# Performance work log

Measured on AMD Instinct MI355X. Metric: run time of the kernel, lower is better.

The kernel has to match this reference:

```python
import jax, jax.numpy as jnp
import numpy as np

BN_EPS = 1e-5
SLOPE = 0.01  # LeakyReLU negative slope (torch default)


def setup_inputs() -> dict:
    key = jax.random.key(0)
    ks = jax.random.split(key, 16)
    N, E = 100000, 1600000
    Cin, C, S, L, Lc = 64, 128, 256, 3, 2
    inp = {}
    inp["x"] = jax.random.normal(ks[0], (N, Cin), jnp.float32)
    inp["edge_index"] = jax.random.randint(ks[1], (2, E), 0, N, jnp.int32)
    inp["batch"] = jnp.zeros((N,), jnp.int32)
    # first GIN layer params
    inp["eps1"] = jnp.zeros((1,), jnp.float32)
    inp["W1"] = jax.random.normal(ks[2], (Cin, C), jnp.float32) * (1.0 / np.sqrt(Cin))
    inp["b1"] = jnp.zeros((C,), jnp.float32)
    inp["g1"] = jnp.ones((C,), jnp.float32)
    inp["be1"] = jnp.zeros((C,), jnp.float32)
    inp["m1"] = jnp.zeros((C,), jnp.float32)
    inp["v1"] = jax.random.uniform(ks[3], (C,), jnp.float32, 0.5, 1.5)
    # stacked GIN layers
    inp["epsL"] = jnp.zeros((L,), jnp.float32)
    inp["WL"] = jax.random.normal(ks[4], (L, C, C), jnp.float32) * (1.0 / np.sqrt(C))
    inp["bL"] = jnp.zeros((L, C), jnp.float32)
    inp["gL"] = jnp.ones((L, C), jnp.float32)
    inp["beL"] = jnp.zeros((L, C), jnp.float32)
    inp["mL"] = jnp.zeros((L, C), jnp.float32)
    inp["vL"] = jax.random.uniform(ks[5], (L, C), jnp.float32, 0.5, 1.5)
    # classifier
    inp["Wc1"] = jax.random.normal(ks[6], (C, S), jnp.float32) * (1.0 / np.sqrt(C))
    inp["bc1"] = jnp.zeros((S,), jnp.float32)
    inp["Wcl"] = jax.random.normal(ks[7], (Lc, S, S), jnp.float32) * (1.0 / np.sqrt(S))
    inp["bcl"] = jnp.zeros((Lc, S), jnp.float32)
    inp["Wf"] = jax.random.normal(ks[8], (S, 1), jnp.float32) * (1.0 / np.sqrt(S))
    inp["bf"] = jnp.zeros((1,), jnp.float32)
    return inp


def reference(x, edge_index, batch, eps1, W1, b1, g1, be1, m1, v1,
              epsL, WL, bL, gL, beL, mL, vL, Wc1, bc1, Wcl, bcl, Wf, bf):
    N = x.shape[0]
    src, dst = edge_index[0], edge_index[1]
    lrelu = lambda z: jnp.where(z >= 0, z, SLOPE * z)

    def gin(h, eps, W, b, g, be, m, v):
        # scatter-add neighbor aggregation: aggr[i] = sum_{(j->i) in E} h[j]
        aggr = jax.ops.segment_sum(h[src], dst, num_segments=N)
        z = ((1.0 + eps) * h + aggr) @ W + b          # Linear
        z = (z - m) * (g * jax.lax.rsqrt(v + BN_EPS)) + be  # BatchNorm (inference)
        return lrelu(z)                                # LeakyReLU in MLP; Dropout=identity

    h = lrelu(gin(x, eps1, W1, b1, g1, be1, m1, v1))  # outer leaky_relu in forward
    for i in range(WL.shape[0]):
        h = lrelu(gin(h, epsL[i], WL[i], bL[i], gL[i], beL[i], mL[i], vL[i]))
    h = h @ Wc1 + bc1
    for i in range(Wcl.shape[0]):
        h = lrelu(h @ Wcl[i] + bcl[i])
    return jax.nn.sigmoid(h @ Wf + bf)  # [N, 1]
```

## Files before the change

### kernel.cpp

```cpp
#include <hip/hip_runtime.h>
#include <stdint.h>


#define NN  100000
#define EE  1600000
#define CIN 64
#define CC  128
#define NBK 782
#define CHUNK 8192
#define NCH 196

typedef __attribute__((ext_vector_type(8))) __bf16 bf16x8;
typedef __attribute__((ext_vector_type(4))) float  f32x4;

__device__ __forceinline__ float bf2f(uint32_t u) { return __uint_as_float(u << 16); }
__device__ __forceinline__ float bf2f_hi(uint32_t u) { return __uint_as_float(u & 0xffff0000u); }
__device__ __forceinline__ ushort f2bf(float f) {
  uint32_t u = __float_as_uint(f);
  u += 0x7fffu + ((u >> 16) & 1u);
  return (ushort)(u >> 16);
}

template<int ACT> __device__ __forceinline__ float actf(float z) {
  if constexpr (ACT == 1) return z >= 0.f ? z : 0.01f * z;
  else if constexpr (ACT == 2) return z >= 0.f ? z : 1e-4f * z;
  else return z;
}

__device__ __forceinline__ void gload_lds16(const void* g, void* l) {
  __builtin_amdgcn_global_load_lds(
      (const __attribute__((address_space(1))) void*)g,
      (__attribute__((address_space(3))) void*)l, 16, 0, 0);
}

__global__ __launch_bounds__(256) void ms_hist_kernel(const int* __restrict__ ei,
                                                      int* __restrict__ hist,
                                                      int* __restrict__ bh, int e) {
  __shared__ int h[NBK];
  for (int i = threadIdx.x; i < NBK; i += 256) h[i] = 0;
  __syncthreads();
  const int base = blockIdx.x * CHUNK;
  const int end = min(base + CHUNK, e);
  for (int i = base + threadIdx.x; i < end; i += 256)
    atomicAdd(&h[ei[e + i] >> 7], 1);
  __syncthreads();
  for (int i = threadIdx.x; i < NBK; i += 256) {
    hist[blockIdx.x * NBK + i] = h[i];
    if (h[i]) atomicAdd(&bh[i], h[i]);
  }
}

__global__ __launch_bounds__(256) void bkt_scan_kernel(const int* __restrict__ bh,
                                                       int* __restrict__ boff, int e) {
  __shared__ int sd[256];
  int t = threadIdx.x;
  int base = t * 4;
  int v0 = base + 0 < NBK ? bh[base + 0] : 0;
  int v1 = base + 1 < NBK ? bh[base + 1] : 0;
  int v2 = base + 2 < NBK ? bh[base + 2] : 0;
  int v3 = base + 3 < NBK ? bh[base + 3] : 0;
  int ts = v0 + v1 + v2 + v3;
  sd[t] = ts; __syncthreads();
  for (int off = 1; off < 256; off <<= 1) {
    int u = (t >= off) ? sd[t - off] : 0;
    __syncthreads();
    sd[t] += u;
    __syncthreads();
  }
  int excl = sd[t] - ts;
  if (base + 0 < NBK) boff[base + 0] = excl;
  if (base + 1 < NBK) boff[base + 1] = excl + v0;
  if (base + 2 < NBK) boff[base + 2] = excl + v0 + v1;
  if (base + 3 < NBK) boff[base + 3] = excl + v0 + v1 + v2;
  if (t == 255) boff[NBK] = e;
}

__global__ void ms_offs_kernel(int* __restrict__ hist, const int* __restrict__ boff) {
  int b = blockIdx.x * 256 + threadIdx.x;
  if (b >= NBK) return;
  int run = boff[b];
  for (int k = 0; k < NCH; ++k) {
    int t = hist[k * NBK + b];
    hist[k * NBK + b] = run;
    run += t;
  }
}

__global__ __launch_bounds__(256) void ms_scatter_kernel(const int* __restrict__ ei,
                                                         const int* __restrict__ hist,
                                                         uint* __restrict__ ebkt, int e) {
  __shared__ int cur[NBK];
  for (int i = threadIdx.x; i < NBK; i += 256) cur[i] = hist[blockIdx.x * NBK + i];
  __syncthreads();
  const int base = blockIdx.x * CHUNK;
  const int end = min(base + CHUNK, e);
  for (int i = base + threadIdx.x; i < end; i += 256) {
    int s = ei[i], d = ei[e + i];
    int p = atomicAdd(&cur[d >> 7], 1);
    ebkt[p] = ((uint)(d & 127) << 17) | (uint)s;
  }
}

__global__ __launch_bounds__(256) void bkt_deg_kernel(const uint* __restrict__ ebkt,
                                                      const int* __restrict__ boff,
                                                      int* __restrict__ deg, int n) {
  __shared__ int dl[128];
  int b = blockIdx.x;
  for (int i = threadIdx.x; i < 128; i += 256) dl[i] = 0;
  __syncthreads();
  int j1 = boff[b + 1];
  for (int j = boff[b] + threadIdx.x; j < j1; j += 256)
    atomicAdd(&dl[ebkt[j] >> 17], 1);
  __syncthreads();
  for (int i = threadIdx.x; i < 128; i += 256) {
    int node = (b << 7) + i;
    if (node < n) deg[node] = dl[i];
  }
}

__global__ __launch_bounds__(256) void bkt_fill_kernel(const uint* __restrict__ ebkt,
                                                       const int* __restrict__ boff,
                                                       const int* __restrict__ rowp,
                                                       int* __restrict__ colb, int n) {
  __shared__ int cur[128];
  int b = blockIdx.x;
  for (int i = threadIdx.x; i < 128; i += 256) {
    int node = (b << 7) + i;
    cur[i] = (node < n) ? rowp[node] : 0;
  }
  __syncthreads();
  int j1 = boff[b + 1];
  for (int j = boff[b] + threadIdx.x; j < j1; j += 256) {
    uint v = ebkt[j];
    int p = atomicAdd(&cur[v >> 17], 1);
    colb[p] = (int)(v & 0x1FFFFu);
  }
}

__global__ void scan1_kernel(const int* __restrict__ deg, int* __restrict__ outp,
                             int* __restrict__ partial, int n) {
  __shared__ int sd[256];
  int t = threadIdx.x;
  int base = blockIdx.x * 1024 + t * 4;
  int v0 = base + 0 < n ? deg[base + 0] : 0;
  int v1 = base + 1 < n ? deg[base + 1] : 0;
  int v2 = base + 2 < n ? deg[base + 2] : 0;
  int v3 = base + 3 < n ? deg[base + 3] : 0;
  int ts = v0 + v1 + v2 + v3;
  sd[t] = ts; __syncthreads();
  for (int off = 1; off < 256; off <<= 1) {
    int u = (t >= off) ? sd[t - off] : 0;
    __syncthreads();
    sd[t] += u;
    __syncthreads();
  }
  int excl = sd[t] - ts;
  if (base + 0 < n) outp[base + 0] = excl;
  if (base + 1 < n) outp[base + 1] = excl + v0;
  if (base + 2 < n) outp[base + 2] = excl + v0 + v1;
  if (base + 3 < n) outp[base + 3] = excl + v0 + v1 + v2;
  if (t == 255) partial[blockIdx.x] = sd[255];
}

__global__ void scan2_kernel(int* __restrict__ partial, int nb) {
  __shared__ int sd[256];
  int t = threadIdx.x;
  int v = t < nb ? partial[t] : 0;
  sd[t] = v; __syncthreads();
  for (int off = 1; off < 256; off <<= 1) {
    int u = (t >= off) ? sd[t - off] : 0;
    __syncthreads();
    sd[t] += u;
    __syncthreads();
  }
  if (t < nb) partial[t] = sd[t] - v;
}

__global__ void scan3_kernel(int* __restrict__ rowp, const int* __restrict__ partial,
                             int n, int e) {
  int i = blockIdx.x * 256 + threadIdx.x;
  if (i == 0) rowp[n] = e;
  if (i < n) rowp[i] += partial[i >> 10];
}

__global__ void bnprep_kernel(const float* b1, const float* g1, const float* be1,
                              const float* m1, const float* v1,
                              const float* bL, const float* gL, const float* beL,
                              const float* mL, const float* vL,
                              float* __restrict__ sc, float* __restrict__ tc) {
  int i = blockIdx.x * 256 + threadIdx.x;
  if (i >= 4 * 128) return;
  int layer = i >> 7, c = i & 127;
  float b, g, be, m, v;
  if (layer == 0) { b = b1[c]; g = g1[c]; be = be1[c]; m = m1[c]; v = v1[c]; }
  else { int o = (layer - 1) * 128 + c; b = bL[o]; g = gL[o]; be = beL[o]; m = mL[o]; v = vL[o]; }
  float s = g * rsqrtf(v + 1e-5f);
  sc[i] = s;
  tc[i] = (b - m) * s + be;
}

__global__ void wtprep_kernel(const float* __restrict__ W1, const float* __restrict__ WL,
                              const float* __restrict__ Wc1, const float* __restrict__ Wcl,
                              ushort* __restrict__ wt1, ushort* __restrict__ wtL,
                              ushort* __restrict__ wtc1, ushort* __restrict__ wtcl) {
  int i = blockIdx.x * 256 + threadIdx.x;
  if (i < 8192) {
    int m = i >> 6, k = i & 63;
    wt1[i] = f2bf(W1[k * 128 + m]);
  } else if (i < 8192 + 49152) {
    int j = i - 8192;
    int l = j >> 14, r = j & 16383, m = r >> 7, k = r & 127;
    wtL[j] = f2bf(WL[l * 16384 + k * 128 + m]);
  } else if (i < 8192 + 49152 + 32768) {
    int j = i - (8192 + 49152);
    int m = j >> 7, k = j & 127;
    wtc1[j] = f2bf(Wc1[k * 256 + m]);
  } else if (i < 8192 + 49152 + 32768 + 131072) {
    int j = i - (8192 + 49152 + 32768);
    int l = j >> 16, r = j & 65535, m = r >> 8, k = r & 255;
    wtcl[j] = f2bf(Wcl[l * 65536 + k * 256 + m]);
  }
}

__global__ void xconv_kernel(const float* __restrict__ x, ushort* __restrict__ xb, int n4) {
  int i = blockIdx.x * 256 + threadIdx.x;
  if (i < n4) {
    float4 v = ((const float4*)x)[i];
    ushort4 o;
    o.x = f2bf(v.x); o.y = f2bf(v.y); o.z = f2bf(v.z); o.w = f2bf(v.w);
    ((ushort4*)xb)[i] = o;
  }
}

template<int C>
__global__ __launch_bounds__(256) void agg_kernel(
    const ushort* __restrict__ hb, const int* __restrict__ rowp,
    const int* __restrict__ colb, const float* __restrict__ ep,
    ushort* __restrict__ zout, int n)
{
  constexpr int LPE = C / 8;
  constexpr int EPR = 64 / LPE;
  const int lane = threadIdx.x & 63;
  const int node = blockIdx.x * 4 + (threadIdx.x >> 6);
  if (node >= n) return;
  const float e1 = 1.0f + ep[0];
  const int lo = lane & (LPE - 1);
  const int g  = lane / LPE;
  int j0 = rowp[node], jend = rowp[node + 1];

  float a0 = 0.f, a1 = 0.f, a2 = 0.f, a3 = 0.f,
        a4 = 0.f, a5 = 0.f, a6 = 0.f, a7 = 0.f;

  for (; j0 < jend; j0 += 64) {
    int cnt = jend - j0; if (cnt > 64) cnt = 64;
    int myn = (lane < cnt) ? colb[j0 + lane] : 0;
    int rounds = (cnt + EPR - 1) / EPR;
    #pragma unroll 4
    for (int r = 0; r < rounds; ++r) {
      int e = r * EPR + g;
      int u = __shfl(myn, e);
      if (e < cnt) {
        const uint4 v = *(const uint4*)(hb + (size_t)u * C + lo * 8);
        a0 += bf2f(v.x); a1 += bf2f_hi(v.x);
        a2 += bf2f(v.y); a3 += bf2f_hi(v.y);
        a4 += bf2f(v.z); a5 += bf2f_hi(v.z);
        a6 += bf2f(v.w); a7 += bf2f_hi(v.w);
      }
    }
  }

  #pragma unroll
  for (int s = LPE; s < 64; s <<= 1) {
    a0 += __shfl_xor(a0, s); a1 += __shfl_xor(a1, s);
    a2 += __shfl_xor(a2, s); a3 += __shfl_xor(a3, s);
    a4 += __shfl_xor(a4, s); a5 += __shfl_xor(a5, s);
    a6 += __shfl_xor(a6, s); a7 += __shfl_xor(a7, s);
  }

  if (g == 0) {
    const uint4 d = *(const uint4*)(hb + (size_t)node * C + lo * 8);
    uint4 o;
    o.x = (uint)f2bf(e1 * bf2f(d.x) + a0) | ((uint)f2bf(e1 * bf2f_hi(d.x) + a1) << 16);
    o.y = (uint)f2bf(e1 * bf2f(d.y) + a2) | ((uint)f2bf(e1 * bf2f_hi(d.y) + a3) << 16);
    o.z = (uint)f2bf(e1 * bf2f(d.z) + a4) | ((uint)f2bf(e1 * bf2f_hi(d.z) + a5) << 16);
    o.w = (uint)f2bf(e1 * bf2f(d.w) + a6) | ((uint)f2bf(e1 * bf2f_hi(d.w) + a7) << 16);
    *(uint4*)(zout + (size_t)node * C + lo * 8) = o;
  }
}

template<int K, int M, int ACT, bool BN>
__global__ __launch_bounds__(256) void gemm_kernel(
    const ushort* __restrict__ xin,
    const ushort* __restrict__ wt,
    const float*  __restrict__ sc,
    const float*  __restrict__ tc,
    ushort* __restrict__ hout,
    int n)
{
  constexpr int KS = 64;
  __shared__ ushort ldsW[128 * KS];
  __shared__ ushort ldsX[128 * KS];
  const int tid = threadIdx.x;
  const int wave = tid >> 6, lane = tid & 63;
  const int lr = lane & 15, lg = lane >> 4;
  const int n0 = blockIdx.x * 128;
  const int mB = blockIdx.y * 128;

  f32x4 acc[8][2];
  #pragma unroll
  for (int r = 0; r < 8; ++r) {
    acc[r][0] = (f32x4){0.f, 0.f, 0.f, 0.f};
    acc[r][1] = (f32x4){0.f, 0.f, 0.f, 0.f};
  }

  #pragma unroll
  for (int s = 0; s < K / KS; ++s) {
    if (s) __syncthreads();
    #pragma unroll
    for (int i = 0; i < 4; ++i) {
      const int ub = wave * 4096 + i * 1024;
      const int a  = ub + lane * 16;
      const int m  = a >> 7;
      const int o  = (a & 127) ^ ((m & 7) << 4);
      gload_lds16((const char*)wt + ((size_t)(mB + m) * K) * 2 + s * 128 + o,
                  (char*)ldsW + ub);
      int nd = n0 + m; if (nd >= n) nd = n - 1;
      gload_lds16((const char*)xin + ((size_t)nd * K) * 2 + s * 128 + o,
                  (char*)ldsX + ub);
    }
    asm volatile("s_waitcnt vmcnt(0)" ::: "memory");
    __syncthreads();
    #pragma unroll
    for (int k0 = 0; k0 < KS; k0 += 32) {
      const int kb = (k0 + lg * 8) * 2;
      bf16x8 wf0, wf1;
      {
        int m = wave * 32 + lr;
        wf0 = __builtin_bit_cast(bf16x8,
              *(const uint4*)((const char*)ldsW + ((m * 128 + kb) ^ ((m & 7) << 4))));
        m += 16;
        wf1 = __builtin_bit_cast(bf16x8,
              *(const uint4*)((const char*)ldsW + ((m * 128 + kb) ^ ((m & 7) << 4))));
      }
      #pragma unroll
      for (int r = 0; r < 8; ++r) {
        int xr = r * 16 + lr;
        bf16x8 xf = __builtin_bit_cast(bf16x8,
              *(const uint4*)((const char*)ldsX + ((xr * 128 + kb) ^ ((xr & 7) << 4))));
        acc[r][0] = __builtin_amdgcn_mfma_f32_16x16x32_bf16(wf0, xf, acc[r][0], 0, 0, 0);
        acc[r][1] = __builtin_amdgcn_mfma_f32_16x16x32_bf16(wf1, xf, acc[r][1], 0, 0, 0);
      }
    }
  }

  #pragma unroll
  for (int ct = 0; ct < 2; ++ct) {
    const int c0 = mB + wave * 32 + ct * 16 + lg * 4;
    float4 sv;
    if constexpr (BN) sv = *(const float4*)(sc + c0);
    else sv = make_float4(1.f, 1.f, 1.f, 1.f);
    const float4 tv = *(const float4*)(tc + c0);
    #pragma unroll
    for (int r = 0; r < 8; ++r) {
      const int node = n0 + r * 16 + lr;
      if (node < n) {
        const f32x4 a = acc[r][ct];
        ushort4 o;
        o.x = f2bf(actf<ACT>(a[0] * sv.x + tv.x));
        o.y = f2bf(actf<ACT>(a[1] * sv.y + tv.y));
        o.z = f2bf(actf<ACT>(a[2] * sv.z + tv.z));
        o.w = f2bf(actf<ACT>(a[3] * sv.w + tv.w));
        *(ushort4*)(hout + (size_t)node * M + c0) = o;
      }
    }
  }
}

__global__ __launch_bounds__(512) void cls_kernel(
    const ushort* __restrict__ xin,
    const ushort* __restrict__ wc1,
    const float*  __restrict__ bc1,
    const ushort* __restrict__ wcl,
    const float*  __restrict__ bcl,
    const float*  __restrict__ wfv,
    const float*  __restrict__ bfp,
    float* __restrict__ out, int n)
{
  extern __shared__ char lds[];
  char* ldsW0 = lds;
  char* ldsW1 = lds + 32768;
  char* ldsH  = lds + 65536;
  char* ldsX  = lds + 131072;
  const int tid = threadIdx.x;
  const int wave = tid >> 6, lane = tid & 63;
  const int lr = lane & 15, lg = lane >> 4;
  const int n0 = blockIdx.x * 128;

  f32x4 acc[8][2];

  auto stageW = [&](const ushort* wsrc, int K2, int s, char* dst) {
    #pragma unroll
    for (int i = 0; i < 4; ++i) {
      const int ub = wave * 4096 + i * 1024;
      const int a = ub + lane * 16;
      const int m = a >> 7;
      const int o = (a & 127) ^ ((m & 7) << 4);
      gload_lds16((const char*)wsrc + (size_t)m * K2 * 2 + s * 128 + o, dst + ub);
    }
  };
  auto stageX = [&](int s) {
    #pragma unroll
    for (int i = 0; i < 2; ++i) {
      const int ub = wave * 2048 + i * 1024;
      const int a = ub + lane * 16;
      const int m = a >> 7;
      const int o = (a & 127) ^ ((m & 7) << 4);
      int nd = n0 + m; if (nd >= n) nd = n - 1;
      gload_lds16((const char*)xin + (size_t)nd * 128 * 2 + s * 128 + o, ldsX + ub);
    }
  };
  auto mfma_slab = [&](const char* wbuf, const char* xbase, int rowOff) {
    #pragma unroll
    for (int k0 = 0; k0 < 64; k0 += 32) {
      const int kb = (k0 + lg * 8) * 2;
      bf16x8 wfr[2];
      #pragma unroll
      for (int ct = 0; ct < 2; ++ct) {
        int m = wave * 32 + ct * 16 + lr;
        wfr[ct] = __builtin_bit_cast(bf16x8,
                  *(const uint4*)(wbuf + ((m * 128 + kb) ^ ((m & 7) << 4))));
      }
      #pragma unroll
      for (int r = 0; r < 8; ++r) {
        int xr = rowOff + r * 16 + lr;
        bf16x8 xf = __builtin_bit_cast(bf16x8,
                    *(const uint4*)(xbase + ((xr * 128 + kb) ^ ((xr & 7) << 4))));
        #pragma unroll
        for (int ct = 0; ct < 2; ++ct)
          acc[r][ct] = __builtin_amdgcn_mfma_f32_16x16x32_bf16(wfr[ct], xf, acc[r][ct], 0, 0, 0);
      }
    }
  };
  auto zacc = [&]() {
    #pragma unroll
    for (int r = 0; r < 8; ++r)
      #pragma unroll
      for (int c = 0; c < 2; ++c) acc[r][c] = (f32x4){0.f, 0.f, 0.f, 0.f};
  };
  auto writeH = [&](const float* bias, bool act) {
    #pragma unroll
    for (int ct = 0; ct < 2; ++ct) {
      const int c0 = wave * 32 + ct * 16 + lg * 4;
      const float4 bv = *(const float4*)(bias + c0);
      const int slab = c0 >> 6, cis = (c0 & 63) * 2;
      #pragma unroll
      for (int r = 0; r < 8; ++r) {
        const int rowH = slab * 128 + r * 16 + lr;
        const f32x4 a = acc[r][ct];
        ushort4 o;
        if (act) {
          o.x = f2bf(actf<1>(a[0] + bv.x)); o.y = f2bf(actf<1>(a[1] + bv.y));
          o.z = f2bf(actf<1>(a[2] + bv.z)); o.w = f2bf(actf<1>(a[3] + bv.w));
        } else {
          o.x = f2bf(a[0] + bv.x); o.y = f2bf(a[1] + bv.y);
          o.z = f2bf(a[2] + bv.z); o.w = f2bf(a[3] + bv.w);
        }
        *(ushort4*)(ldsH + ((rowH * 128 + cis) ^ ((rowH & 7) << 4))) = o;
      }
    }
  };

  zacc();
  #pragma unroll
  for (int s = 0; s < 2; ++s) {
    if (s) __syncthreads();
    stageX(s);
    stageW(wc1, 128, s, ldsW0);
    asm volatile("s_waitcnt vmcnt(0)" ::: "memory");
    __syncthreads();
    mfma_slab(ldsW0, ldsX, 0);
  }
  __syncthreads();
  writeH(bc1, false);

  for (int g = 0; g < 2; ++g) {
    const ushort* Wg = wcl + g * 65536;
    const float*  bg = bcl + g * 256;
    zacc();
    __syncthreads();
    stageW(Wg, 256, 0, ldsW0);
    #pragma unroll
    for (int s = 0; s < 4; ++s) {
      char* cur = (s & 1) ? ldsW1 : ldsW0;
      char* nxt = (s & 1) ? ldsW0 : ldsW1;
      if (s + 1 < 4) {
        stageW(Wg, 256, s + 1, nxt);
        asm volatile("s_waitcnt vmcnt(4)" ::: "memory");
      } else {
        asm volatile("s_waitcnt vmcnt(0)" ::: "memory");
      }
      __syncthreads();
      mfma_slab(cur, ldsH, s * 128);
      __syncthreads();
    }
    if (g == 0) {
      writeH(bg, true);
    } else {
      float* red = (float*)ldsX;
      #pragma unroll
      for (int r = 0; r < 8; ++r) {
        float p = 0.f;
        #pragma unroll
        for (int ct = 0; ct < 2; ++ct) {
          const int c0 = wave * 32 + ct * 16 + lg * 4;
          const float4 bv = *(const float4*)(bg + c0);
          const float4 wv = *(const float4*)(wfv + c0);
          const f32x4 a = acc[r][ct];
          p += actf<1>(a[0] + bv.x) * wv.x + actf<1>(a[1] + bv.y) * wv.y
             + actf<1>(a[2] + bv.z) * wv.z + actf<1>(a[3] + bv.w) * wv.w;
        }
        p += __shfl_xor(p, 16);
        p += __shfl_xor(p, 32);
        if (lg == 0) red[wave * 128 + r * 16 + lr] = p;
      }
      __syncthreads();
      if (tid < 128) {
        const int nd = n0 + tid;
        if (nd < n) {
          float logit = bfp[0];
          #pragma unroll
          for (int w = 0; w < 8; ++w) logit += red[w * 128 + tid];
          out[nd] = 1.f / (1.f + expf(-logit));
        }
      }
    }
  }
}

extern "C" void kernel_launch(void* const* d_in, const int* in_sizes, int n_in,
                              void* d_out, int out_size, void* d_ws, size_t ws_size,
                              hipStream_t stream)
{
  const float* x    = (const float*)d_in[0];
  const int*   ei   = (const int*)d_in[1];
  const float* eps1 = (const float*)d_in[3];
  const float* W1   = (const float*)d_in[4];
  const float* b1   = (const float*)d_in[5];
  const float* g1   = (const float*)d_in[6];
  const float* be1  = (const float*)d_in[7];
  const float* m1   = (const float*)d_in[8];
  const float* v1   = (const float*)d_in[9];
  const float* epsL = (const float*)d_in[10];
  const float* WL   = (const float*)d_in[11];
  const float* bL   = (const float*)d_in[12];
  const float* gL   = (const float*)d_in[13];
  const float* beL  = (const float*)d_in[14];
  const float* mL   = (const float*)d_in[15];
  const float* vL   = (const float*)d_in[16];
  const float* Wc1  = (const float*)d_in[17];
  const float* bc1  = (const float*)d_in[18];
  const float* Wcl  = (const float*)d_in[19];
  const float* bcl  = (const float*)d_in[20];
  const float* Wf   = (const float*)d_in[21];
  const float* bfp  = (const float*)d_in[22];
  float* out = (float*)d_out;

  char* w = (char*)d_ws;
  size_t off = 0;
  auto alloc = [&](size_t bytes) {
    char* p = w + off;
    off += (bytes + 255) & ~(size_t)255;
    return p;
  };
  ushort* bufA   = (ushort*)alloc((size_t)NN * 256 * 2);
  ushort* bufB   = (ushort*)alloc((size_t)NN * 256 * 2);
  int*    rowp   = (int*)alloc((NN + 1) * 4);
  int*    deg    = (int*)alloc(NN * 4);
  int*    colb   = (int*)alloc((size_t)EE * 4);
  uint*   ebkt   = (uint*)alloc((size_t)EE * 4);
  int*    hist   = (int*)alloc((size_t)NCH * NBK * 4);
  int*    bh     = (int*)alloc(NBK * 4);
  int*    boff   = (int*)alloc((NBK + 1) * 4);
  int*    partial= (int*)alloc(1024);
  ushort* wt1    = (ushort*)alloc(8192 * 2);
  ushort* wtL    = (ushort*)alloc(49152 * 2);
  ushort* wtc1   = (ushort*)alloc(32768 * 2);
  ushort* wtcl   = (ushort*)alloc(131072 * 2);
  float*  sc     = (float*)alloc(512 * 4);
  float*  tc     = (float*)alloc(512 * 4);
  (void)ws_size; (void)in_sizes; (void)n_in; (void)out_size;

  hipMemsetAsync(bh, 0, NBK * 4, stream);
  ms_hist_kernel<<<NCH, 256, 0, stream>>>(ei, hist, bh, EE);
  bkt_scan_kernel<<<1, 256, 0, stream>>>(bh, boff, EE);
  ms_offs_kernel<<<(NBK + 255) / 256, 256, 0, stream>>>(hist, boff);
  ms_scatter_kernel<<<NCH, 256, 0, stream>>>(ei, hist, ebkt, EE);
  bkt_deg_kernel<<<NBK, 256, 0, stream>>>(ebkt, boff, deg, NN);
  scan1_kernel<<<98, 256, 0, stream>>>(deg, rowp, partial, NN);
  scan2_kernel<<<1, 256, 0, stream>>>(partial, 98);
  scan3_kernel<<<(NN + 255) / 256, 256, 0, stream>>>(rowp, partial, NN, EE);
  bkt_fill_kernel<<<NBK, 256, 0, stream>>>(ebkt, boff, rowp, colb, NN);

  bnprep_kernel<<<2, 256, 0, stream>>>(b1, g1, be1, m1, v1, bL, gL, beL, mL, vL, sc, tc);
  wtprep_kernel<<<864, 256, 0, stream>>>(W1, WL, Wc1, Wcl, wt1, wtL, wtc1, wtcl);
  xconv_kernel<<<(NN * CIN / 4 + 255) / 256, 256, 0, stream>>>(x, bufA, NN * CIN / 4);

  const int GB = (NN + 127) / 128;

  agg_kernel<64><<<25000, 256, 0, stream>>>(bufA, rowp, colb, eps1, bufB, NN);
  gemm_kernel<64, 128, 2, true><<<dim3(GB, 1), 256, 0, stream>>>(bufB, wt1, sc, tc, bufA, NN);
  for (int i = 0; i < 3; ++i) {
    agg_kernel<128><<<25000, 256, 0, stream>>>(bufA, rowp, colb, epsL + i, bufB, NN);
    gemm_kernel<128, 128, 2, true><<<dim3(GB, 1), 256, 0, stream>>>(
        bufB, wtL + i * 16384, sc + 128 * (i + 1), tc + 128 * (i + 1), bufA, NN);
  }
  hipFuncSetAttribute(reinterpret_cast<const void*>(cls_kernel),
                      hipFuncAttributeMaxDynamicSharedMemorySize, 147456);
  cls_kernel<<<GB, 512, 147456, stream>>>(bufA, wtc1, bc1, wtcl, bcl, Wf, bfp, out, NN);
}
```

Measured before the change: 455.0 us.

## Store node features in FP8 (bf8) for neighbor aggregation gathers

Node feature tensors that feed the gather-based aggregation are now stored in 8-bit bf8 (e5m2) format instead of bf16. This halves the bytes per random neighbor gather. The input conversion and the GEMM epilogues write bf8, and the aggregation decodes it with hardware packed conversions when available. The final GIN layer still writes bf16 for the classifier. The cost is a large loss of precision (a 2-bit mantissa) on the activations, which may break accuracy tolerance.

```diff
diff --git a/kernel.cpp b/kernel.cpp
--- a/kernel.cpp
+++ b/kernel.cpp
@@ -1,4 +1,5 @@
 #include <hip/hip_runtime.h>
+#include <hip/hip_fp16.h>
 #include <stdint.h>
 
 
@@ -12,6 +13,7 @@
 
 typedef __attribute__((ext_vector_type(8))) __bf16 bf16x8;
 typedef __attribute__((ext_vector_type(4))) float  f32x4;
+typedef __attribute__((ext_vector_type(2))) float  f32x2;
 
 __device__ __forceinline__ float bf2f(uint32_t u) { return __uint_as_float(u << 16); }
 __device__ __forceinline__ float bf2f_hi(uint32_t u) { return __uint_as_float(u & 0xffff0000u); }
@@ -19,6 +21,35 @@
   uint32_t u = __float_as_uint(f);
   u += 0x7fffu + ((u >> 16) & 1u);
   return (ushort)(u >> 16);
+}
+
+#if __has_builtin(__builtin_amdgcn_cvt_pk_f32_bf8) && __has_builtin(__builtin_amdgcn_cvt_pk_bf8_f32)
+#define F8_HW 1
+#endif
+
+template<bool HI> __device__ __forceinline__ f32x2 dec_pk(uint d) {
+#ifdef F8_HW
+  return __builtin_amdgcn_cvt_pk_f32_bf8((int)d, HI);
+#else
+  uint w = HI ? (d >> 16) : d;
+  f32x2 r;
+  uint b0 = w & 0xFFu, b1 = (w >> 8) & 0xFFu;
+  r.x = __uint_as_float(((b0 & 0x80u) << 24) | ((b0 & 0x7Fu) << 21)) * 0x1.0p112f;
+  r.y = __uint_as_float(((b1 & 0x80u) << 24) | ((b1 & 0x7Fu) << 21)) * 0x1.0p112f;
+  return r;
+#endif
+}
+template<bool HI> __device__ __forceinline__ uint enc_pk(float a, float b, uint old) {
+#ifdef F8_HW
+  return (uint)__builtin_amdgcn_cvt_pk_bf8_f32(a, b, (int)old, HI);
+#else
+  ushort ha = __half_as_ushort(__float2half(a));
+  ushort hb = __half_as_ushort(__float2half(b));
+  ha = (ushort)(ha + 0x7F + ((ha >> 8) & 1));
+  hb = (ushort)(hb + 0x7F + ((hb >> 8) & 1));
+  uint two = (uint)(ha >> 8) | ((uint)(hb >> 8) << 8);
+  return HI ? ((old & 0x0000FFFFu) | (two << 16)) : ((old & 0xFFFF0000u) | two);
+#endif
 }
 
 template<int ACT> __device__ __forceinline__ float actf(float z) {
@@ -222,23 +253,23 @@
   }
 }
 
-__global__ void xconv_kernel(const float* __restrict__ x, ushort* __restrict__ xb, int n4) {
+__global__ void xconv_kernel(const float* __restrict__ x, uchar* __restrict__ x8, int n4) {
   int i = blockIdx.x * 256 + threadIdx.x;
   if (i < n4) {
     float4 v = ((const float4*)x)[i];
-    ushort4 o;
-    o.x = f2bf(v.x); o.y = f2bf(v.y); o.z = f2bf(v.z); o.w = f2bf(v.w);
-    ((ushort4*)xb)[i] = o;
+    uint w = enc_pk<false>(v.x, v.y, 0u);
+    w = enc_pk<true>(v.z, v.w, w);
+    ((uint*)x8)[i] = w;
   }
 }
 
 template<int C>
 __global__ __launch_bounds__(256) void agg_kernel(
-    const ushort* __restrict__ hb, const int* __restrict__ rowp,
+    const uchar* __restrict__ hb8, const int* __restrict__ rowp,
     const int* __restrict__ colb, const float* __restrict__ ep,
     ushort* __restrict__ zout, int n)
 {
-  constexpr int LPE = C / 8;
+  constexpr int LPE = C / 16;
   constexpr int EPR = 64 / LPE;
   const int lane = threadIdx.x & 63;
   const int node = blockIdx.x * 4 + (threadIdx.x >> 6);
@@ -248,8 +279,9 @@
   const int g  = lane / LPE;
   int j0 = rowp[node], jend = rowp[node + 1];
 
-  float a0 = 0.f, a1 = 0.f, a2 = 0.f, a3 = 0.f,
-        a4 = 0.f, a5 = 0.f, a6 = 0.f, a7 = 0.f;
+  float a[16];
+  #pragma unroll
+  for (int i = 0; i < 16; ++i) a[i] = 0.f;
 
   for (; j0 < jend; j0 += 64) {
     int cnt = jend - j0; if (cnt > 64) cnt = 64;
@@ -260,41 +292,52 @@
       int e = r * EPR + g;
       int u = __shfl(myn, e);
       if (e < cnt) {
-        const uint4 v = *(const uint4*)(hb + (size_t)u * C + lo * 8);
-        a0 += bf2f(v.x); a1 += bf2f_hi(v.x);
-        a2 += bf2f(v.y); a3 += bf2f_hi(v.y);
-        a4 += bf2f(v.z); a5 += bf2f_hi(v.z);
-        a6 += bf2f(v.w); a7 += bf2f_hi(v.w);
+        const uint4 v = *(const uint4*)(hb8 + (size_t)u * C + lo * 16);
+        f32x2 p;
+        p = dec_pk<false>(v.x); a[0] += p.x;  a[1] += p.y;
+        p = dec_pk<true >(v.x); a[2] += p.x;  a[3] += p.y;
+        p = dec_pk<false>(v.y); a[4] += p.x;  a[5] += p.y;
+        p = dec_pk<true >(v.y); a[6] += p.x;  a[7] += p.y;
+        p = dec_pk<false>(v.z); a[8] += p.x;  a[9] += p.y;
+        p = dec_pk<true >(v.z); a[10] += p.x; a[11] += p.y;
+        p = dec_pk<false>(v.w); a[12] += p.x; a[13] += p.y;
+        p = dec_pk<true >(v.w); a[14] += p.x; a[15] += p.y;
       }
     }
   }
 
   #pragma unroll
-  for (int s = LPE; s < 64; s <<= 1) {
-    a0 += __shfl_xor(a0, s); a1 += __shfl_xor(a1, s);
-    a2 += __shfl_xor(a2, s); a3 += __shfl_xor(a3, s);
-    a4 += __shfl_xor(a4, s); a5 += __shfl_xor(a5, s);
-    a6 += __shfl_xor(a6, s); a7 += __shfl_xor(a7, s);
-  }
+  for (int s = LPE; s < 64; s <<= 1)
+    #pragma unroll
+    for (int i = 0; i < 16; ++i) a[i] += __shfl_xor(a[i], s);
 
   if (g == 0) {
-    const uint4 d = *(const uint4*)(hb + (size_t)node * C + lo * 8);
-    uint4 o;
-    o.x = (uint)f2bf(e1 * bf2f(d.x) + a0) | ((uint)f2bf(e1 * bf2f_hi(d.x) + a1) << 16);
-    o.y = (uint)f2bf(e1 * bf2f(d.y) + a2) | ((uint)f2bf(e1 * bf2f_hi(d.y) + a3) << 16);
-    o.z = (uint)f2bf(e1 * bf2f(d.z) + a4) | ((uint)f2bf(e1 * bf2f_hi(d.z) + a5) << 16);
-    o.w = (uint)f2bf(e1 * bf2f(d.w) + a6) | ((uint)f2bf(e1 * bf2f_hi(d.w) + a7) << 16);
-    *(uint4*)(zout + (size_t)node * C + lo * 8) = o;
-  }
-}
-
-template<int K, int M, int ACT, bool BN>
+    const uint4 d = *(const uint4*)(hb8 + (size_t)node * C + lo * 16);
+    float sv[16];
+    f32x2 p;
+    p = dec_pk<false>(d.x); sv[0] = p.x;  sv[1] = p.y;
+    p = dec_pk<true >(d.x); sv[2] = p.x;  sv[3] = p.y;
+    p = dec_pk<false>(d.y); sv[4] = p.x;  sv[5] = p.y;
+    p = dec_pk<true >(d.y); sv[6] = p.x;  sv[7] = p.y;
+    p = dec_pk<false>(d.z); sv[8] = p.x;  sv[9] = p.y;
+    p = dec_pk<true >(d.z); sv[10] = p.x; sv[11] = p.y;
+    p = dec_pk<false>(d.w); sv[12] = p.x; sv[13] = p.y;
+    p = dec_pk<true >(d.w); sv[14] = p.x; sv[15] = p.y;
+    ushort r[16];
+    #pragma unroll
+    for (int i = 0; i < 16; ++i) r[i] = f2bf(e1 * sv[i] + a[i]);
+    *(uint4*)(zout + (size_t)node * C + lo * 16)     = *(uint4*)&r[0];
+    *(uint4*)(zout + (size_t)node * C + lo * 16 + 8) = *(uint4*)&r[8];
+  }
+}
+
+template<int K, int M, int ACT, bool BN, bool F8OUT>
 __global__ __launch_bounds__(256) void gemm_kernel(
     const ushort* __restrict__ xin,
     const ushort* __restrict__ wt,
     const float*  __restrict__ sc,
     const float*  __restrict__ tc,
-    ushort* __restrict__ hout,
+    void* __restrict__ hout,
     int n)
 {
   constexpr int KS = 64;
@@ -365,12 +408,19 @@
       const int node = n0 + r * 16 + lr;
       if (node < n) {
         const f32x4 a = acc[r][ct];
-        ushort4 o;
-        o.x = f2bf(actf<ACT>(a[0] * sv.x + tv.x));
-        o.y = f2bf(actf<ACT>(a[1] * sv.y + tv.y));
-        o.z = f2bf(actf<ACT>(a[2] * sv.z + tv.z));
-        o.w = f2bf(actf<ACT>(a[3] * sv.w + tv.w));
-        *(ushort4*)(hout + (size_t)node * M + c0) = o;
+        float v0 = actf<ACT>(a[0] * sv.x + tv.x);
+        float v1 = actf<ACT>(a[1] * sv.y + tv.y);
+        float v2 = actf<ACT>(a[2] * sv.z + tv.z);
+        float v3 = actf<ACT>(a[3] * sv.w + tv.w);
+        if constexpr (F8OUT) {
+          uint wv = enc_pk<false>(v0, v1, 0u);
+          wv = enc_pk<true>(v2, v3, wv);
+          *(uint*)((uchar*)hout + (size_t)node * M + c0) = wv;
+        } else {
+          ushort4 o;
+          o.x = f2bf(v0); o.y = f2bf(v1); o.z = f2bf(v2); o.w = f2bf(v3);
+          *(ushort4*)((ushort*)hout + (size_t)node * M + c0) = o;
+        }
       }
     }
   }
@@ -574,6 +624,7 @@
   };
   ushort* bufA   = (ushort*)alloc((size_t)NN * 256 * 2);
   ushort* bufB   = (ushort*)alloc((size_t)NN * 256 * 2);
+  uchar*  h8     = (uchar*)alloc((size_t)NN * 128);
   int*    rowp   = (int*)alloc((NN + 1) * 4);
   int*    deg    = (int*)alloc(NN * 4);
   int*    colb   = (int*)alloc((size_t)EE * 4);
@@ -603,17 +654,20 @@
 
   bnprep_kernel<<<2, 256, 0, stream>>>(b1, g1, be1, m1, v1, bL, gL, beL, mL, vL, sc, tc);
   wtprep_kernel<<<864, 256, 0, stream>>>(W1, WL, Wc1, Wcl, wt1, wtL, wtc1, wtcl);
-  xconv_kernel<<<(NN * CIN / 4 + 255) / 256, 256, 0, stream>>>(x, bufA, NN * CIN / 4);
+  xconv_kernel<<<(NN * CIN / 4 + 255) / 256, 256, 0, stream>>>(x, h8, NN * CIN / 4);
 
   const int GB = (NN + 127) / 128;
 
-  agg_kernel<64><<<25000, 256, 0, stream>>>(bufA, rowp, colb, eps1, bufB, NN);
-  gemm_kernel<64, 128, 2, true><<<dim3(GB, 1), 256, 0, stream>>>(bufB, wt1, sc, tc, bufA, NN);
-  for (int i = 0; i < 3; ++i) {
-    agg_kernel<128><<<25000, 256, 0, stream>>>(bufA, rowp, colb, epsL + i, bufB, NN);
-    gemm_kernel<128, 128, 2, true><<<dim3(GB, 1), 256, 0, stream>>>(
-        bufB, wtL + i * 16384, sc + 128 * (i + 1), tc + 128 * (i + 1), bufA, NN);
-  }
+  agg_kernel<64><<<25000, 256, 0, stream>>>(h8, rowp, colb, eps1, bufB, NN);
+  gemm_kernel<64, 128, 2, true, true><<<dim3(GB, 1), 256, 0, stream>>>(bufB, wt1, sc, tc, h8, NN);
+  for (int i = 0; i < 2; ++i) {
+    agg_kernel<128><<<25000, 256, 0, stream>>>(h8, rowp, colb, epsL + i, bufB, NN);
+    gemm_kernel<128, 128, 2, true, true><<<dim3(GB, 1), 256, 0, stream>>>(
+        bufB, wtL + i * 16384, sc + 128 * (i + 1), tc + 128 * (i + 1), h8, NN);
+  }
+  agg_kernel<128><<<25000, 256, 0, stream>>>(h8, rowp, colb, epsL + 2, bufB, NN);
+  gemm_kernel<128, 128, 2, true, false><<<dim3(GB, 1), 256, 0, stream>>>(
+      bufB, wtL + 2 * 16384, sc + 128 * 3, tc + 128 * 3, bufA, NN);
   hipFuncSetAttribute(reinterpret_cast<const void*>(cls_kernel),
                       hipFuncAttributeMaxDynamicSharedMemorySize, 147456);
   cls_kernel<<<GB, 512, 147456, stream>>>(bufA, wtc1, bc1, wtcl, bcl, Wf, bfp, out, NN);
```

Measured after the change: 457.5 us. About the same (+0.6%).
